# Kernel tuning notes

Hardware: AMD Instinct MI355X
Metric: run time of the kernel (lower is better)

## Reference

```python
import jax, jax.numpy as jnp
import numpy as np

N_NODES = 50000
N_EDGES = 800000
IN_DIM = 128
HID_DIM = 64
OUT_DIM = 40
N_REL = 8


def setup_inputs() -> dict:
    key = jax.random.key(0)
    ks = jax.random.split(key, 12)
    x = jax.random.normal(ks[0], (N_NODES, IN_DIM), dtype=jnp.float32)
    edge_index = jax.random.randint(ks[1], (2, N_EDGES), 0, N_NODES, dtype=jnp.int64)
    edge_type = jax.random.randint(ks[2], (N_EDGES,), 0, N_REL, dtype=jnp.int64)
    s = 0.05
    W1 = jax.random.normal(ks[3], (N_REL, IN_DIM, HID_DIM), dtype=jnp.float32) * s
    root1 = jax.random.normal(ks[4], (IN_DIM, HID_DIM), dtype=jnp.float32) * s
    b1 = jnp.zeros((HID_DIM,), dtype=jnp.float32)
    W2 = jax.random.normal(ks[5], (N_REL, HID_DIM, HID_DIM), dtype=jnp.float32) * s
    root2 = jax.random.normal(ks[6], (HID_DIM, HID_DIM), dtype=jnp.float32) * s
    b2 = jnp.zeros((HID_DIM,), dtype=jnp.float32)
    Wl = jax.random.normal(ks[7], (HID_DIM, OUT_DIM), dtype=jnp.float32) * s
    bl = jnp.zeros((OUT_DIM,), dtype=jnp.float32)
    return {"x": x, "edge_index": edge_index, "edge_type": edge_type,
            "W1": W1, "root1": root1, "b1": b1,
            "W2": W2, "root2": root2, "b2": b2,
            "Wl": Wl, "bl": bl}


def _rgcn_conv(x, W, Wroot, b, src, dst, edge_type):
    # PyG RGCNConv (no bases/blocks, aggr='mean'):
    #   out[i] = sum_r mean_{(j->i) of rel r} (x[j] @ W[r]) + x[i] @ Wroot + b
    N = x.shape[0]
    R = W.shape[0]
    h = jnp.einsum('ni,rio->rno', x, W)        # [R, N, out]
    msgs = h[edge_type, src]                   # [E, out] edge gather
    seg = edge_type * N + dst                  # per (relation, dst) segment
    sums = jax.ops.segment_sum(msgs, seg, num_segments=R * N)
    cnt = jax.ops.segment_sum(jnp.ones((msgs.shape[0],), x.dtype), seg,
                              num_segments=R * N)
    mean = sums / jnp.maximum(cnt, 1.0)[:, None]
    agg = mean.reshape(R, N, -1).sum(axis=0)   # sum over relations
    return agg + x @ Wroot + b


def reference(x, edge_index, edge_type, W1, root1, b1, W2, root2, b2, Wl, bl):
    src, dst = edge_index[0], edge_index[1]
    h = jax.nn.relu(_rgcn_conv(x, W1, root1, b1, src, dst, edge_type))
    # dropout is identity in eval mode
    h = jax.nn.relu(_rgcn_conv(h, W2, root2, b2, src, dst, edge_type))
    logits = h @ Wl + bl
    return jax.nn.log_softmax(logits, axis=1)
```

## Files before the change

kernel.cpp:

```cpp
#include <hip/hip_runtime.h>
#include <hip/hip_bf16.h>
#include <cmath>

#define IN_DIM 128
#define HID 64
#define OUT_DIM 40
#define NREL 8
#define NCOLS 576
#define CAP 64
#define CSTR 16

typedef __attribute__((ext_vector_type(8))) short short8;
typedef __attribute__((ext_vector_type(4))) short short4v;
typedef __attribute__((ext_vector_type(4))) float floatx4;
typedef __attribute__((ext_vector_type(2))) float f32x2;

static __device__ __forceinline__ short f2bf(float f) {
  __hip_bfloat16 h = __float2bfloat16(f);
  return __builtin_bit_cast(short, h);
}
static __device__ __forceinline__ float bflo(unsigned int u) {
  return __int_as_float(u << 16);
}
static __device__ __forceinline__ float bfhi(unsigned int u) {
  return __int_as_float(u & 0xffff0000u);
}
static __device__ __forceinline__ unsigned int packbf(float x, float y) {
  unsigned int lo = (unsigned short)f2bf(x);
  unsigned int hi = (unsigned short)f2bf(y);
  return lo | (hi << 16);
}

__global__ void pack_zero(const float* __restrict__ W1, const float* __restrict__ root1,
                          short* __restrict__ Bt1,
                          const float* __restrict__ W2, const float* __restrict__ root2,
                          short* __restrict__ Bt2,
                          int4* __restrict__ curv, int nz) {
  const int PB1 = (NCOLS * IN_DIM + 255) / 256;
  const int PB2 = (NCOLS * HID + 255) / 256;
  int b = blockIdx.x;
  if (b < PB1) {
    int i = b * 256 + threadIdx.x;
    if (i >= NCOLS * IN_DIM) return;
    int c = i / IN_DIM, k = i % IN_DIM;
    float v = (c < NREL * HID)
      ? W1[((size_t)(c >> 6) * IN_DIM + k) * HID + (c & 63)]
      : root1[(size_t)k * HID + (c - NREL * HID)];
    Bt1[i] = f2bf(v);
  } else if (b < PB1 + PB2) {
    int i = (b - PB1) * 256 + threadIdx.x;
    if (i >= NCOLS * HID) return;
    int c = i / HID, k = i % HID;
    float v = (c < NREL * HID)
      ? W2[((size_t)(c >> 6) * HID + k) * HID + (c & 63)]
      : root2[(size_t)k * HID + (c - NREL * HID)];
    Bt2[i] = f2bf(v);
  } else {
    int i = (b - PB1 - PB2) * 256 + threadIdx.x;
    if (i < nz) curv[i] = make_int4(0, 0, 0, 0);
  }
}

template<int K, int AMODE>
__device__ __forceinline__ void gemm_dev(
    short* As, short* Bs,
    const void* __restrict__ Aptr, const short* __restrict__ Bt,
    const float* __restrict__ bias, short* __restrict__ H,
    unsigned short* __restrict__ AGG, int M, int row0)
{
  constexpr int AST = K + 8;
  int tid = threadIdx.x;
  int wv = tid >> 6, lane = tid & 63;
  int lm = lane & 15, quad = lane >> 4;

  if (AMODE == 0) {
    const float* A = (const float*)Aptr;
    constexpr int CH = K / 4;
    for (int i = tid; i < 64 * CH; i += 256) {
      int r = i / CH, kq = i % CH;
      int gr = row0 + r; if (gr >= M) gr = M - 1;
      float4 v = *(const float4*)(A + (unsigned)(gr * K + kq * 4));
      short4v s;
      s.x = f2bf(v.x); s.y = f2bf(v.y); s.z = f2bf(v.z); s.w = f2bf(v.w);
      *(short4v*)(As + r * AST + kq * 4) = s;
    }
  } else {
    const short* A = (const short*)Aptr;
    constexpr int CH = K / 8;
    for (int i = tid; i < 64 * CH; i += 256) {
      int r = i / CH, ko = i % CH;
      int gr = row0 + r; if (gr >= M) gr = M - 1;
      short8 v = *(const short8*)(A + (unsigned)(gr * K + ko * 8));
      #pragma unroll
      for (int j = 0; j < 8; ++j)
        if ((unsigned short)v[j] & 0x8000u) v[j] = 0;
      *(short8*)(As + r * AST + ko * 8) = v;
    }
  }

  const short* ap = As + (16 * wv + lm) * AST + quad * 8;

  for (int cy = 0; cy < 9; ++cy) {
    constexpr int CB = K / 8;
    for (int i = tid; i < 64 * CB; i += 256) {
      int n = i / CB, ko = i % CB;
      short8 v = *(const short8*)(Bt + (unsigned)((cy * 64 + n) * K + ko * 8));
      *(short8*)(Bs + n * AST + ko * 8) = v;
    }
    __syncthreads();

    floatx4 acc[4] = {{0,0,0,0},{0,0,0,0},{0,0,0,0},{0,0,0,0}};
    #pragma unroll
    for (int ks = 0; ks < K / 32; ++ks) {
      short8 a = *(const short8*)(ap + ks * 32);
      #pragma unroll
      for (int nb = 0; nb < 4; ++nb) {
        short8 b = *(const short8*)(Bs + (nb * 16 + lm) * AST + ks * 32 + quad * 8);
        acc[nb] = __builtin_amdgcn_mfma_f32_16x16x32_bf16(a, b, acc[nb], 0, 0, 0);
      }
    }
    __syncthreads();

    int mbase = row0 + 16 * wv + quad * 4;
    if (cy < 8) {
      #pragma unroll
      for (int nb = 0; nb < 4; ++nb) {
        int col = cy * 64 + nb * 16 + lm;
        #pragma unroll
        for (int r = 0; r < 4; ++r) {
          int mg = mbase + r;
          if (mg < M) H[(unsigned)mg * (NREL * HID) + col] = f2bf(acc[nb][r]);
        }
      }
    } else {
      #pragma unroll
      for (int nb = 0; nb < 4; ++nb) {
        int col = nb * 16 + lm;
        float bv = bias[col];
        #pragma unroll
        for (int r = 0; r < 4; ++r) {
          int mg = mbase + r;
          if (mg < M)
            AGG[(unsigned)mg * HID + col] = (unsigned short)f2bf(acc[nb][r] + bv);
        }
      }
    }
  }
}

__global__ __launch_bounds__(256, 4) void gemm1_scatter(
    const float* __restrict__ A, const short* __restrict__ Bt,
    const float* __restrict__ bias, short* __restrict__ H,
    unsigned short* __restrict__ AGG, int M, int GB,
    const int* __restrict__ src, const int* __restrict__ dst,
    const int* __restrict__ et,
    int* __restrict__ cursor, int* __restrict__ ev, int E)
{
  constexpr int AST = IN_DIM + 8;
  __shared__ short As[64 * AST];
  __shared__ short Bs[64 * AST];
  if ((int)blockIdx.x < GB) {
    gemm_dev<IN_DIM, 0>(As, Bs, A, Bt, bias, H, AGG, M, blockIdx.x * 64);
  } else {
    int e = (blockIdx.x - GB) * 256 + threadIdx.x;
    if (e >= E) return;
    int d = dst[e];
    int pos = atomicAdd(&cursor[d * CSTR], 1);
    if (pos < CAP)
      __builtin_nontemporal_store((src[e] << 3) | et[e], &ev[d * CAP + pos]);
  }
}

__global__ __launch_bounds__(256, 4) void gemm2_mfma(
    const unsigned short* __restrict__ A, const short* __restrict__ Bt,
    const float* __restrict__ bias, short* __restrict__ H,
    unsigned short* __restrict__ AGG, int M)
{
  constexpr int AST = HID + 8;
  __shared__ short As[64 * AST];
  __shared__ short Bs[64 * AST];
  gemm_dev<HID, 1>(As, Bs, A, Bt, bias, H, AGG, M, blockIdx.x * 64);
}

static __device__ __forceinline__ void agg_core(
    const uint2* __restrict__ Hu2, const int* __restrict__ evrow,
    int cnt, int lane, int q, int sub,
    float& a0, float& a1, float& a2, float& a3)
{
  int ew = evrow[lane];
  int t = ew & 7;
  float wt = 0.f;
  #pragma unroll
  for (int r = 0; r < 8; ++r) {
    unsigned long long m = __ballot(lane < cnt && t == r);
    int c = __popcll(m);
    if (t == r) wt = 1.0f / (float)(c > 1 ? c : 1);
  }
  f32x2 A01 = {a0, a1}, A23 = {a2, a3};
  int npass = (cnt + 31) >> 5;
  for (int P = 0; P < npass; ++P) {
    int base = P * 32 + q * 8;
    int ee[8]; float ww[8];
    #pragma unroll
    for (int i = 0; i < 8; ++i) {
      int j = base + i;
      int jj = j < cnt ? j : cnt - 1;
      ee[i] = __shfl(ew, jj, 64);
      float w = __shfl(wt, jj, 64);
      ww[i] = (j < cnt) ? w : 0.f;
    }
    uint2 hv[8];
    #pragma unroll
    for (int i = 0; i < 8; ++i)
      hv[i] = Hu2[(unsigned)ee[i] * 16u + (unsigned)sub];
    #pragma unroll
    for (int i = 0; i < 8; ++i) {
      f32x2 w2 = {ww[i], ww[i]};
      f32x2 h01 = {bflo(hv[i].x), bfhi(hv[i].x)};
      f32x2 h23 = {bflo(hv[i].y), bfhi(hv[i].y)};
      A01 += h01 * w2;
      A23 += h23 * w2;
    }
  }
  a0 = A01.x; a1 = A01.y; a2 = A23.x; a3 = A23.y;
  a0 += __shfl_xor(a0, 16, 64); a0 += __shfl_xor(a0, 32, 64);
  a1 += __shfl_xor(a1, 16, 64); a1 += __shfl_xor(a1, 32, 64);
  a2 += __shfl_xor(a2, 16, 64); a2 += __shfl_xor(a2, 32, 64);
  a3 += __shfl_xor(a3, 16, 64); a3 += __shfl_xor(a3, 32, 64);
}

__global__ __launch_bounds__(256) void csr_agg(
    const short* __restrict__ H, const int* __restrict__ cursor,
    const int* __restrict__ ev, unsigned short* __restrict__ AGG, int N)
{
  int d = blockIdx.x * 4 + (threadIdx.x >> 6);
  if (d >= N) return;
  int lane = threadIdx.x & 63;
  int q = lane >> 4, sub = lane & 15;
  int cnt = cursor[d * CSTR]; if (cnt > CAP) cnt = CAP;
  float a0 = 0.f, a1 = 0.f, a2 = 0.f, a3 = 0.f;
  uint2* aggrow = (uint2*)(AGG + (size_t)d * HID);
  if (q == 0) {
    uint2 iv = aggrow[sub];
    a0 = bflo(iv.x); a1 = bfhi(iv.x); a2 = bflo(iv.y); a3 = bfhi(iv.y);
  }
  if (cnt > 0)
    agg_core((const uint2*)H, ev + d * CAP, cnt, lane, q, sub, a0, a1, a2, a3);
  if (q == 0) {
    uint2 ov;
    ov.x = packbf(a0, a1);
    ov.y = packbf(a2, a3);
    aggrow[sub] = ov;
  }
}

__global__ __launch_bounds__(256) void csr_agg_final(
    const short* __restrict__ H, const int* __restrict__ cursor,
    const int* __restrict__ ev, const unsigned short* __restrict__ AGG,
    const float* __restrict__ Wl, const float* __restrict__ bl,
    float* __restrict__ out, int N)
{
  __shared__ float sWl[HID * OUT_DIM];
  __shared__ float sbl[OUT_DIM];
  __shared__ float sh[4][HID];
  int tid = threadIdx.x;
  for (int i = tid; i < HID * OUT_DIM; i += 256) sWl[i] = Wl[i];
  if (tid < OUT_DIM) sbl[tid] = bl[tid];
  __syncthreads();

  int wv = tid >> 6, lane = tid & 63;
  int q = lane >> 4, sub = lane & 15;
  int d = blockIdx.x * 4 + wv;
  bool valid = d < N;
  int dc = valid ? d : (N - 1);

  int cnt = cursor[dc * CSTR]; if (cnt > CAP) cnt = CAP;
  float a0 = 0.f, a1 = 0.f, a2 = 0.f, a3 = 0.f;
  if (q == 0) {
    uint2 iv = ((const uint2*)(AGG + (size_t)dc * HID))[sub];
    a0 = bflo(iv.x); a1 = bfhi(iv.x); a2 = bflo(iv.y); a3 = bfhi(iv.y);
  }
  if (cnt > 0)
    agg_core((const uint2*)H, ev + dc * CAP, cnt, lane, q, sub, a0, a1, a2, a3);
  if (q == 0) {
    float4 v;
    v.x = fmaxf(a0, 0.f); v.y = fmaxf(a1, 0.f);
    v.z = fmaxf(a2, 0.f); v.w = fmaxf(a3, 0.f);
    *(float4*)(&sh[wv][4 * sub]) = v;
  }
  __syncthreads();

  float logit = -__builtin_inff();
  if (lane < OUT_DIM) {
    float t = sbl[lane];
    #pragma unroll 8
    for (int k = 0; k < HID; ++k) t += sh[wv][k] * sWl[k * OUT_DIM + lane];
    logit = t;
  }
  float m = logit;
  #pragma unroll
  for (int o = 32; o > 0; o >>= 1) m = fmaxf(m, __shfl_xor(m, o, 64));
  float ex = (lane < OUT_DIM) ? expf(logit - m) : 0.f;
  float s = ex;
  #pragma unroll
  for (int o = 32; o > 0; o >>= 1) s += __shfl_xor(s, o, 64);
  if (valid && lane < OUT_DIM)
    out[(size_t)d * OUT_DIM + lane] = logit - m - logf(s);
}

extern "C" void kernel_launch(void* const* d_in, const int* in_sizes, int n_in,
                              void* d_out, int out_size, void* d_ws, size_t ws_size,
                              hipStream_t stream) {
  const float* x     = (const float*)d_in[0];
  const int*   eidx  = (const int*)d_in[1];
  const int*   etype = (const int*)d_in[2];
  const float* W1    = (const float*)d_in[3];
  const float* root1 = (const float*)d_in[4];
  const float* b1    = (const float*)d_in[5];
  const float* W2    = (const float*)d_in[6];
  const float* root2 = (const float*)d_in[7];
  const float* b2    = (const float*)d_in[8];
  const float* Wl    = (const float*)d_in[9];
  const float* bl    = (const float*)d_in[10];

  int N = in_sizes[0] / IN_DIM;
  int E = in_sizes[2];
  const int* srcp = eidx;
  const int* dstp = eidx + E;

  char* ws = (char*)d_ws;
  size_t off = 0;
  auto alloc = [&](size_t bytes) -> char* {
    char* p = ws + off;
    off += (bytes + 255) & ~(size_t)255;
    return p;
  };
  short* Bt1    = (short*)alloc((size_t)NCOLS * IN_DIM * 2);
  short* Bt2    = (short*)alloc((size_t)NCOLS * HID * 2);
  int*   cursor = (int*)alloc((size_t)N * CSTR * 4);
  int*   ev     = (int*)alloc((size_t)N * CAP * 4);
  short* H      = (short*)alloc((size_t)N * NREL * HID * 2);
  unsigned short* AGG1 = (unsigned short*)alloc((size_t)N * HID * 2);
  unsigned short* AGG2 = (unsigned short*)alloc((size_t)N * HID * 2);

  const int PB1 = (NCOLS * IN_DIM + 255) / 256;
  const int PB2 = (NCOLS * HID + 255) / 256;
  int nz = N * CSTR / 4;
  int ZB = (nz + 255) / 256;
  pack_zero<<<PB1 + PB2 + ZB, 256, 0, stream>>>(W1, root1, Bt1, W2, root2, Bt2,
                                                (int4*)cursor, nz);

  int GB = (N + 63) / 64;
  int SB = (E + 255) / 256;
  gemm1_scatter<<<GB + SB, 256, 0, stream>>>(x, Bt1, b1, H, AGG1, N, GB,
                                             srcp, dstp, etype, cursor, ev, E);

  csr_agg<<<(N + 3) / 4, 256, 0, stream>>>(H, cursor, ev, AGG1, N);
  gemm2_mfma<<<GB, 256, 0, stream>>>(AGG1, Bt2, b2, H, AGG2, N);
  csr_agg_final<<<(N + 3) / 4, 256, 0, stream>>>(H, cursor, ev, AGG2,
                                                 Wl, bl, (float*)d_out, N);
}
```

Baseline: 233.3 us.

## Fuse layer-1 aggregation into layer-2 GEMM and precompute edge weight codes

Removes the standalone csr_agg kernel. The second GEMM now gathers neighbours for its own 64-row tile, applies ReLU and writes the aggregated rows straight into shared memory, so the AGG1 round trip through global memory goes away. A new finalize_ev pass packs each edge's per-relation count code into the edge list once. Both aggregation paths then get their mean weights from a small reciprocal lookup table and read edge entries with vector loads, instead of recomputing ballots and shuffles every time. The trade-off is a gather phase with much less parallelism: each wave handles 16 rows serially inside only about 782 GEMM blocks. It also adds an extra kernel launch and a second H buffer, and AGG1 is reused as AGG2.

```diff
diff --git a/kernel.cpp b/kernel.cpp
--- a/kernel.cpp
+++ b/kernel.cpp
@@ -61,41 +61,26 @@
   }
 }
 
-template<int K, int AMODE>
-__device__ __forceinline__ void gemm_dev(
+__device__ __forceinline__ void gemm1_dev(
     short* As, short* Bs,
-    const void* __restrict__ Aptr, const short* __restrict__ Bt,
+    const float* __restrict__ A, const short* __restrict__ Bt,
     const float* __restrict__ bias, short* __restrict__ H,
     unsigned short* __restrict__ AGG, int M, int row0)
 {
+  constexpr int K = IN_DIM;
   constexpr int AST = K + 8;
   int tid = threadIdx.x;
   int wv = tid >> 6, lane = tid & 63;
   int lm = lane & 15, quad = lane >> 4;
 
-  if (AMODE == 0) {
-    const float* A = (const float*)Aptr;
-    constexpr int CH = K / 4;
-    for (int i = tid; i < 64 * CH; i += 256) {
-      int r = i / CH, kq = i % CH;
-      int gr = row0 + r; if (gr >= M) gr = M - 1;
-      float4 v = *(const float4*)(A + (unsigned)(gr * K + kq * 4));
-      short4v s;
-      s.x = f2bf(v.x); s.y = f2bf(v.y); s.z = f2bf(v.z); s.w = f2bf(v.w);
-      *(short4v*)(As + r * AST + kq * 4) = s;
-    }
-  } else {
-    const short* A = (const short*)Aptr;
-    constexpr int CH = K / 8;
-    for (int i = tid; i < 64 * CH; i += 256) {
-      int r = i / CH, ko = i % CH;
-      int gr = row0 + r; if (gr >= M) gr = M - 1;
-      short8 v = *(const short8*)(A + (unsigned)(gr * K + ko * 8));
-      #pragma unroll
-      for (int j = 0; j < 8; ++j)
-        if ((unsigned short)v[j] & 0x8000u) v[j] = 0;
-      *(short8*)(As + r * AST + ko * 8) = v;
-    }
+  constexpr int CH = K / 4;
+  for (int i = tid; i < 64 * CH; i += 256) {
+    int r = i / CH, kq = i % CH;
+    int gr = row0 + r; if (gr >= M) gr = M - 1;
+    float4 v = *(const float4*)(A + (unsigned)(gr * K + kq * 4));
+    short4v s;
+    s.x = f2bf(v.x); s.y = f2bf(v.y); s.z = f2bf(v.z); s.w = f2bf(v.w);
+    *(short4v*)(As + r * AST + kq * 4) = s;
   }
 
   const short* ap = As + (16 * wv + lm) * AST + quad * 8;
@@ -160,7 +145,7 @@
   __shared__ short As[64 * AST];
   __shared__ short Bs[64 * AST];
   if ((int)blockIdx.x < GB) {
-    gemm_dev<IN_DIM, 0>(As, Bs, A, Bt, bias, H, AGG, M, blockIdx.x * 64);
+    gemm1_dev(As, Bs, A, Bt, bias, H, AGG, M, blockIdx.x * 64);
   } else {
     int e = (blockIdx.x - GB) * 256 + threadIdx.x;
     if (e >= E) return;
@@ -171,48 +156,42 @@
   }
 }
 
-__global__ __launch_bounds__(256, 4) void gemm2_mfma(
-    const unsigned short* __restrict__ A, const short* __restrict__ Bt,
-    const float* __restrict__ bias, short* __restrict__ H,
-    unsigned short* __restrict__ AGG, int M)
-{
-  constexpr int AST = HID + 8;
-  __shared__ short As[64 * AST];
-  __shared__ short Bs[64 * AST];
-  gemm_dev<HID, 1>(As, Bs, A, Bt, bias, H, AGG, M, blockIdx.x * 64);
-}
-
-static __device__ __forceinline__ void agg_core(
-    const uint2* __restrict__ Hu2, const int* __restrict__ evrow,
-    int cnt, int lane, int q, int sub,
-    float& a0, float& a1, float& a2, float& a3)
-{
-  int ew = evrow[lane];
-  int t = ew & 7;
-  float wt = 0.f;
+__global__ __launch_bounds__(256) void finalize_ev(
+    const int* __restrict__ cursor, int* __restrict__ ev, int N)
+{
+  int d = blockIdx.x * 4 + (threadIdx.x >> 6);
+  if (d >= N) return;
+  int lane = threadIdx.x & 63;
+  int cnt = cursor[d * CSTR]; if (cnt > CAP) cnt = CAP;
+  int e = (lane < cnt) ? ev[d * CAP + lane] : 0;
+  int t = e & 7;
+  int code = 64;
   #pragma unroll
   for (int r = 0; r < 8; ++r) {
     unsigned long long m = __ballot(lane < cnt && t == r);
     int c = __popcll(m);
-    if (t == r) wt = 1.0f / (float)(c > 1 ? c : 1);
-  }
+    if (lane < cnt && t == r) code = c - 1;
+  }
+  ev[d * CAP + lane] = (e << 7) | code;
+}
+
+static __device__ __forceinline__ void agg_fast(
+    const uint2* __restrict__ Hu2, const int* __restrict__ evrow,
+    int npass, int q, int sub, const float* __restrict__ lut,
+    float& a0, float& a1, float& a2, float& a3)
+{
   f32x2 A01 = {a0, a1}, A23 = {a2, a3};
-  int npass = (cnt + 31) >> 5;
   for (int P = 0; P < npass; ++P) {
-    int base = P * 32 + q * 8;
-    int ee[8]; float ww[8];
+    const int4* pp = (const int4*)(evrow + P * 32 + q * 8);
+    int4 v0 = pp[0], v1 = pp[1];
+    int vv[8] = {v0.x, v0.y, v0.z, v0.w, v1.x, v1.y, v1.z, v1.w};
+    uint2 hv[8];
+    float ww[8];
     #pragma unroll
     for (int i = 0; i < 8; ++i) {
-      int j = base + i;
-      int jj = j < cnt ? j : cnt - 1;
-      ee[i] = __shfl(ew, jj, 64);
-      float w = __shfl(wt, jj, 64);
-      ww[i] = (j < cnt) ? w : 0.f;
-    }
-    uint2 hv[8];
-    #pragma unroll
-    for (int i = 0; i < 8; ++i)
-      hv[i] = Hu2[(unsigned)ee[i] * 16u + (unsigned)sub];
+      hv[i] = Hu2[(unsigned)(vv[i] >> 7) * 16u + (unsigned)sub];
+      ww[i] = lut[vv[i] & 127];
+    }
     #pragma unroll
     for (int i = 0; i < 8; ++i) {
       f32x2 w2 = {ww[i], ww[i]};
@@ -229,28 +208,97 @@
   a3 += __shfl_xor(a3, 16, 64); a3 += __shfl_xor(a3, 32, 64);
 }
 
-__global__ __launch_bounds__(256) void csr_agg(
-    const short* __restrict__ H, const int* __restrict__ cursor,
-    const int* __restrict__ ev, unsigned short* __restrict__ AGG, int N)
-{
-  int d = blockIdx.x * 4 + (threadIdx.x >> 6);
-  if (d >= N) return;
-  int lane = threadIdx.x & 63;
+__global__ __launch_bounds__(256, 4) void gemm2_fused(
+    const unsigned short* __restrict__ AGG1, const int* __restrict__ cursor,
+    const int* __restrict__ ev, const short* __restrict__ H1,
+    const short* __restrict__ Bt, const float* __restrict__ bias,
+    short* __restrict__ H2, unsigned short* __restrict__ AGG2, int M)
+{
+  constexpr int K = HID;
+  constexpr int AST = K + 8;
+  __shared__ short As[64 * AST];
+  __shared__ short Bs[64 * AST];
+  __shared__ float lut[128];
+
+  int tid = threadIdx.x;
+  if (tid < 128) lut[tid] = (tid < 64) ? 1.0f / (float)(tid + 1) : 0.f;
+  __syncthreads();
+
+  int row0 = blockIdx.x * 64;
+  int wv = tid >> 6, lane = tid & 63;
+  int lm = lane & 15, quad = lane >> 4;
   int q = lane >> 4, sub = lane & 15;
-  int cnt = cursor[d * CSTR]; if (cnt > CAP) cnt = CAP;
-  float a0 = 0.f, a1 = 0.f, a2 = 0.f, a3 = 0.f;
-  uint2* aggrow = (uint2*)(AGG + (size_t)d * HID);
-  if (q == 0) {
-    uint2 iv = aggrow[sub];
-    a0 = bflo(iv.x); a1 = bfhi(iv.x); a2 = bflo(iv.y); a3 = bfhi(iv.y);
-  }
-  if (cnt > 0)
-    agg_core((const uint2*)H, ev + d * CAP, cnt, lane, q, sub, a0, a1, a2, a3);
-  if (q == 0) {
-    uint2 ov;
-    ov.x = packbf(a0, a1);
-    ov.y = packbf(a2, a3);
-    aggrow[sub] = ov;
+
+  for (int j = 0; j < 16; ++j) {
+    int r = wv * 16 + j;
+    int d = row0 + r;
+    int dc = d < M ? d : M - 1;
+    int cnt = cursor[dc * CSTR]; if (cnt > CAP) cnt = CAP;
+    float a0 = 0.f, a1 = 0.f, a2 = 0.f, a3 = 0.f;
+    if (q == 0) {
+      uint2 iv = ((const uint2*)(AGG1 + (size_t)dc * HID))[sub];
+      a0 = bflo(iv.x); a1 = bfhi(iv.x); a2 = bflo(iv.y); a3 = bfhi(iv.y);
+    }
+    int npass = (cnt + 31) >> 5;
+    if (npass > 0)
+      agg_fast((const uint2*)H1, ev + dc * CAP, npass, q, sub, lut, a0, a1, a2, a3);
+    if (q == 0) {
+      ushort4 o;
+      o.x = (unsigned short)f2bf(fmaxf(a0, 0.f));
+      o.y = (unsigned short)f2bf(fmaxf(a1, 0.f));
+      o.z = (unsigned short)f2bf(fmaxf(a2, 0.f));
+      o.w = (unsigned short)f2bf(fmaxf(a3, 0.f));
+      *(ushort4*)(As + r * AST + sub * 4) = o;
+    }
+  }
+
+  const short* ap = As + (16 * wv + lm) * AST + quad * 8;
+
+  for (int cy = 0; cy < 9; ++cy) {
+    constexpr int CB = K / 8;
+    for (int i = tid; i < 64 * CB; i += 256) {
+      int n = i / CB, ko = i % CB;
+      short8 v = *(const short8*)(Bt + (unsigned)((cy * 64 + n) * K + ko * 8));
+      *(short8*)(Bs + n * AST + ko * 8) = v;
+    }
+    __syncthreads();
+
+    floatx4 acc[4] = {{0,0,0,0},{0,0,0,0},{0,0,0,0},{0,0,0,0}};
+    #pragma unroll
+    for (int ks = 0; ks < K / 32; ++ks) {
+      short8 a = *(const short8*)(ap + ks * 32);
+      #pragma unroll
+      for (int nb = 0; nb < 4; ++nb) {
+        short8 b = *(const short8*)(Bs + (nb * 16 + lm) * AST + ks * 32 + quad * 8);
+        acc[nb] = __builtin_amdgcn_mfma_f32_16x16x32_bf16(a, b, acc[nb], 0, 0, 0);
+      }
+    }
+    __syncthreads();
+
+    int mbase = row0 + 16 * wv + quad * 4;
+    if (cy < 8) {
+      #pragma unroll
+      for (int nb = 0; nb < 4; ++nb) {
+        int col = cy * 64 + nb * 16 + lm;
+        #pragma unroll
+        for (int r = 0; r < 4; ++r) {
+          int mg = mbase + r;
+          if (mg < M) H2[(unsigned)mg * (NREL * HID) + col] = f2bf(acc[nb][r]);
+        }
+      }
+    } else {
+      #pragma unroll
+      for (int nb = 0; nb < 4; ++nb) {
+        int col = nb * 16 + lm;
+        float bv = bias[col];
+        #pragma unroll
+        for (int r = 0; r < 4; ++r) {
+          int mg = mbase + r;
+          if (mg < M)
+            AGG2[(unsigned)mg * HID + col] = (unsigned short)f2bf(acc[nb][r] + bv);
+        }
+      }
+    }
   }
 }
 
@@ -263,9 +311,11 @@
   __shared__ float sWl[HID * OUT_DIM];
   __shared__ float sbl[OUT_DIM];
   __shared__ float sh[4][HID];
+  __shared__ float lut[128];
   int tid = threadIdx.x;
   for (int i = tid; i < HID * OUT_DIM; i += 256) sWl[i] = Wl[i];
   if (tid < OUT_DIM) sbl[tid] = bl[tid];
+  if (tid < 128) lut[tid] = (tid < 64) ? 1.0f / (float)(tid + 1) : 0.f;
   __syncthreads();
 
   int wv = tid >> 6, lane = tid & 63;
@@ -280,8 +330,9 @@
     uint2 iv = ((const uint2*)(AGG + (size_t)dc * HID))[sub];
     a0 = bflo(iv.x); a1 = bfhi(iv.x); a2 = bflo(iv.y); a3 = bfhi(iv.y);
   }
-  if (cnt > 0)
-    agg_core((const uint2*)H, ev + dc * CAP, cnt, lane, q, sub, a0, a1, a2, a3);
+  int npass = (cnt + 31) >> 5;
+  if (npass > 0)
+    agg_fast((const uint2*)H, ev + dc * CAP, npass, q, sub, lut, a0, a1, a2, a3);
   if (q == 0) {
     float4 v;
     v.x = fmaxf(a0, 0.f); v.y = fmaxf(a1, 0.f);
@@ -339,9 +390,10 @@
   short* Bt2    = (short*)alloc((size_t)NCOLS * HID * 2);
   int*   cursor = (int*)alloc((size_t)N * CSTR * 4);
   int*   ev     = (int*)alloc((size_t)N * CAP * 4);
-  short* H      = (short*)alloc((size_t)N * NREL * HID * 2);
+  short* H1     = (short*)alloc((size_t)N * NREL * HID * 2);
+  short* H2     = (short*)alloc((size_t)N * NREL * HID * 2);
   unsigned short* AGG1 = (unsigned short*)alloc((size_t)N * HID * 2);
-  unsigned short* AGG2 = (unsigned short*)alloc((size_t)N * HID * 2);
+  unsigned short* AGG2 = AGG1;
 
   const int PB1 = (NCOLS * IN_DIM + 255) / 256;
   const int PB2 = (NCOLS * HID + 255) / 256;
@@ -352,11 +404,13 @@
 
   int GB = (N + 63) / 64;
   int SB = (E + 255) / 256;
-  gemm1_scatter<<<GB + SB, 256, 0, stream>>>(x, Bt1, b1, H, AGG1, N, GB,
+  gemm1_scatter<<<GB + SB, 256, 0, stream>>>(x, Bt1, b1, H1, AGG1, N, GB,
                                              srcp, dstp, etype, cursor, ev, E);
 
-  csr_agg<<<(N + 3) / 4, 256, 0, stream>>>(H, cursor, ev, AGG1, N);
-  gemm2_mfma<<<GB, 256, 0, stream>>>(AGG1, Bt2, b2, H, AGG2, N);
-  csr_agg_final<<<(N + 3) / 4, 256, 0, stream>>>(H, cursor, ev, AGG2,
+  finalize_ev<<<(N + 3) / 4, 256, 0, stream>>>(cursor, ev, N);
+
+  gemm2_fused<<<GB, 256, 0, stream>>>(AGG1, cursor, ev, H1, Bt2, b2, H2, AGG2, N);
+
+  csr_agg_final<<<(N + 3) / 4, 256, 0, stream>>>(H2, cursor, ev, AGG2,
                                                  Wl, bl, (float*)d_out, N);
 }
```

Result: no change. 237.6 us (+1.9%).

## Precompute per-edge mean weights in first aggregation and reuse in final pass

Applied to the files above, without the earlier changes.

The first aggregation kernel now computes per-relation counts through ballots and writes them back into the edge list, packed with the gather index as a small code. The final aggregation then reads those packed entries with vector loads and looks up 1/count in a shared-memory table, instead of repeating the ballot and shuffle work. Cursor zeroing moves to hipMemsetAsync, and the two layers now write separate H buffers. The cost is an extra write of the edge list and a second large H allocation, and the packed index field shrinks to 25 bits, which still fits the node and relation count.

```diff
diff --git a/kernel.cpp b/kernel.cpp
--- a/kernel.cpp
+++ b/kernel.cpp
@@ -31,13 +31,11 @@
   return lo | (hi << 16);
 }
 
-__global__ void pack_zero(const float* __restrict__ W1, const float* __restrict__ root1,
-                          short* __restrict__ Bt1,
-                          const float* __restrict__ W2, const float* __restrict__ root2,
-                          short* __restrict__ Bt2,
-                          int4* __restrict__ curv, int nz) {
+__global__ void pack_bt(const float* __restrict__ W1, const float* __restrict__ root1,
+                        short* __restrict__ Bt1,
+                        const float* __restrict__ W2, const float* __restrict__ root2,
+                        short* __restrict__ Bt2) {
   const int PB1 = (NCOLS * IN_DIM + 255) / 256;
-  const int PB2 = (NCOLS * HID + 255) / 256;
   int b = blockIdx.x;
   if (b < PB1) {
     int i = b * 256 + threadIdx.x;
@@ -47,7 +45,7 @@
       ? W1[((size_t)(c >> 6) * IN_DIM + k) * HID + (c & 63)]
       : root1[(size_t)k * HID + (c - NREL * HID)];
     Bt1[i] = f2bf(v);
-  } else if (b < PB1 + PB2) {
+  } else {
     int i = (b - PB1) * 256 + threadIdx.x;
     if (i >= NCOLS * HID) return;
     int c = i / HID, k = i % HID;
@@ -55,9 +53,6 @@
       ? W2[((size_t)(c >> 6) * HID + k) * HID + (c & 63)]
       : root2[(size_t)k * HID + (c - NREL * HID)];
     Bt2[i] = f2bf(v);
-  } else {
-    int i = (b - PB1 - PB2) * 256 + threadIdx.x;
-    if (i < nz) curv[i] = make_int4(0, 0, 0, 0);
   }
 }
 
@@ -182,20 +177,38 @@
   gemm_dev<HID, 1>(As, Bs, A, Bt, bias, H, AGG, M, blockIdx.x * 64);
 }
 
-static __device__ __forceinline__ void agg_core(
-    const uint2* __restrict__ Hu2, const int* __restrict__ evrow,
-    int cnt, int lane, int q, int sub,
-    float& a0, float& a1, float& a2, float& a3)
-{
-  int ew = evrow[lane];
+__global__ __launch_bounds__(256) void csr_agg_fe(
+    const short* __restrict__ H, const int* __restrict__ cursor,
+    int* __restrict__ ev, unsigned short* __restrict__ AGG, int N)
+{
+  int d = blockIdx.x * 4 + (threadIdx.x >> 6);
+  if (d >= N) return;
+  int lane = threadIdx.x & 63;
+  int q = lane >> 4, sub = lane & 15;
+  int cnt = cursor[d * CSTR]; if (cnt > CAP) cnt = CAP;
+  int* evrow = ev + d * CAP;
+
+  int ew = (lane < cnt) ? evrow[lane] : 0;
   int t = ew & 7;
+  int code = 64;
   float wt = 0.f;
   #pragma unroll
   for (int r = 0; r < 8; ++r) {
     unsigned long long m = __ballot(lane < cnt && t == r);
     int c = __popcll(m);
-    if (t == r) wt = 1.0f / (float)(c > 1 ? c : 1);
-  }
+    if (lane < cnt && t == r) { code = c - 1; wt = 1.0f / (float)(c > 0 ? c : 1); }
+  }
+  evrow[lane] = (ew << 7) | code;
+
+  float a0, a1, a2, a3;
+  uint2* aggrow = (uint2*)(AGG + (size_t)d * HID);
+  uint2 iv = aggrow[sub];
+  a0 = (q == 0) ? bflo(iv.x) : 0.f;
+  a1 = (q == 0) ? bfhi(iv.x) : 0.f;
+  a2 = (q == 0) ? bflo(iv.y) : 0.f;
+  a3 = (q == 0) ? bfhi(iv.y) : 0.f;
+
+  const uint2* Hu2 = (const uint2*)H;
   f32x2 A01 = {a0, a1}, A23 = {a2, a3};
   int npass = (cnt + 31) >> 5;
   for (int P = 0; P < npass; ++P) {
@@ -227,25 +240,7 @@
   a1 += __shfl_xor(a1, 16, 64); a1 += __shfl_xor(a1, 32, 64);
   a2 += __shfl_xor(a2, 16, 64); a2 += __shfl_xor(a2, 32, 64);
   a3 += __shfl_xor(a3, 16, 64); a3 += __shfl_xor(a3, 32, 64);
-}
-
-__global__ __launch_bounds__(256) void csr_agg(
-    const short* __restrict__ H, const int* __restrict__ cursor,
-    const int* __restrict__ ev, unsigned short* __restrict__ AGG, int N)
-{
-  int d = blockIdx.x * 4 + (threadIdx.x >> 6);
-  if (d >= N) return;
-  int lane = threadIdx.x & 63;
-  int q = lane >> 4, sub = lane & 15;
-  int cnt = cursor[d * CSTR]; if (cnt > CAP) cnt = CAP;
-  float a0 = 0.f, a1 = 0.f, a2 = 0.f, a3 = 0.f;
-  uint2* aggrow = (uint2*)(AGG + (size_t)d * HID);
-  if (q == 0) {
-    uint2 iv = aggrow[sub];
-    a0 = bflo(iv.x); a1 = bfhi(iv.x); a2 = bflo(iv.y); a3 = bfhi(iv.y);
-  }
-  if (cnt > 0)
-    agg_core((const uint2*)H, ev + d * CAP, cnt, lane, q, sub, a0, a1, a2, a3);
+
   if (q == 0) {
     uint2 ov;
     ov.x = packbf(a0, a1);
@@ -254,6 +249,39 @@
   }
 }
 
+static __device__ __forceinline__ void agg_fast(
+    const uint2* __restrict__ Hu2, const int* __restrict__ evrow,
+    int npass, int q, int sub, const float* __restrict__ lut,
+    float& a0, float& a1, float& a2, float& a3)
+{
+  f32x2 A01 = {a0, a1}, A23 = {a2, a3};
+  for (int P = 0; P < npass; ++P) {
+    const int4* pp = (const int4*)(evrow + P * 32 + q * 8);
+    int4 v0 = pp[0], v1 = pp[1];
+    int vv[8] = {v0.x, v0.y, v0.z, v0.w, v1.x, v1.y, v1.z, v1.w};
+    uint2 hv[8];
+    float ww[8];
+    #pragma unroll
+    for (int i = 0; i < 8; ++i) {
+      hv[i] = Hu2[(unsigned)(vv[i] >> 7) * 16u + (unsigned)sub];
+      ww[i] = lut[vv[i] & 127];
+    }
+    #pragma unroll
+    for (int i = 0; i < 8; ++i) {
+      f32x2 w2 = {ww[i], ww[i]};
+      f32x2 h01 = {bflo(hv[i].x), bfhi(hv[i].x)};
+      f32x2 h23 = {bflo(hv[i].y), bfhi(hv[i].y)};
+      A01 += h01 * w2;
+      A23 += h23 * w2;
+    }
+  }
+  a0 = A01.x; a1 = A01.y; a2 = A23.x; a3 = A23.y;
+  a0 += __shfl_xor(a0, 16, 64); a0 += __shfl_xor(a0, 32, 64);
+  a1 += __shfl_xor(a1, 16, 64); a1 += __shfl_xor(a1, 32, 64);
+  a2 += __shfl_xor(a2, 16, 64); a2 += __shfl_xor(a2, 32, 64);
+  a3 += __shfl_xor(a3, 16, 64); a3 += __shfl_xor(a3, 32, 64);
+}
+
 __global__ __launch_bounds__(256) void csr_agg_final(
     const short* __restrict__ H, const int* __restrict__ cursor,
     const int* __restrict__ ev, const unsigned short* __restrict__ AGG,
@@ -263,11 +291,8 @@
   __shared__ float sWl[HID * OUT_DIM];
   __shared__ float sbl[OUT_DIM];
   __shared__ float sh[4][HID];
+  __shared__ float lut[128];
   int tid = threadIdx.x;
-  for (int i = tid; i < HID * OUT_DIM; i += 256) sWl[i] = Wl[i];
-  if (tid < OUT_DIM) sbl[tid] = bl[tid];
-  __syncthreads();
-
   int wv = tid >> 6, lane = tid & 63;
   int q = lane >> 4, sub = lane & 15;
   int d = blockIdx.x * 4 + wv;
@@ -275,13 +300,20 @@
   int dc = valid ? d : (N - 1);
 
   int cnt = cursor[dc * CSTR]; if (cnt > CAP) cnt = CAP;
+  uint2 iv = ((const uint2*)(AGG + (size_t)dc * HID))[sub];
+
+  for (int i = tid; i < HID * OUT_DIM; i += 256) sWl[i] = Wl[i];
+  if (tid < OUT_DIM) sbl[tid] = bl[tid];
+  if (tid < 128) lut[tid] = (tid < 64) ? 1.0f / (float)(tid + 1) : 0.f;
+  __syncthreads();
+
   float a0 = 0.f, a1 = 0.f, a2 = 0.f, a3 = 0.f;
   if (q == 0) {
-    uint2 iv = ((const uint2*)(AGG + (size_t)dc * HID))[sub];
     a0 = bflo(iv.x); a1 = bfhi(iv.x); a2 = bflo(iv.y); a3 = bfhi(iv.y);
   }
-  if (cnt > 0)
-    agg_core((const uint2*)H, ev + dc * CAP, cnt, lane, q, sub, a0, a1, a2, a3);
+  int npass = (cnt + 31) >> 5;
+  if (npass > 0)
+    agg_fast((const uint2*)H, ev + dc * CAP, npass, q, sub, lut, a0, a1, a2, a3);
   if (q == 0) {
     float4 v;
     v.x = fmaxf(a0, 0.f); v.y = fmaxf(a1, 0.f);
@@ -339,24 +371,26 @@
   short* Bt2    = (short*)alloc((size_t)NCOLS * HID * 2);
   int*   cursor = (int*)alloc((size_t)N * CSTR * 4);
   int*   ev     = (int*)alloc((size_t)N * CAP * 4);
-  short* H      = (short*)alloc((size_t)N * NREL * HID * 2);
+  short* H1     = (short*)alloc((size_t)N * NREL * HID * 2);
+  short* H2     = (short*)alloc((size_t)N * NREL * HID * 2);
   unsigned short* AGG1 = (unsigned short*)alloc((size_t)N * HID * 2);
   unsigned short* AGG2 = (unsigned short*)alloc((size_t)N * HID * 2);
 
+  hipMemsetAsync(cursor, 0, (size_t)N * CSTR * 4, stream);
+
   const int PB1 = (NCOLS * IN_DIM + 255) / 256;
   const int PB2 = (NCOLS * HID + 255) / 256;
-  int nz = N * CSTR / 4;
-  int ZB = (nz + 255) / 256;
-  pack_zero<<<PB1 + PB2 + ZB, 256, 0, stream>>>(W1, root1, Bt1, W2, root2, Bt2,
-                                                (int4*)cursor, nz);
+  pack_bt<<<PB1 + PB2, 256, 0, stream>>>(W1, root1, Bt1, W2, root2, Bt2);
 
   int GB = (N + 63) / 64;
   int SB = (E + 255) / 256;
-  gemm1_scatter<<<GB + SB, 256, 0, stream>>>(x, Bt1, b1, H, AGG1, N, GB,
+  gemm1_scatter<<<GB + SB, 256, 0, stream>>>(x, Bt1, b1, H1, AGG1, N, GB,
                                              srcp, dstp, etype, cursor, ev, E);
 
-  csr_agg<<<(N + 3) / 4, 256, 0, stream>>>(H, cursor, ev, AGG1, N);
-  gemm2_mfma<<<GB, 256, 0, stream>>>(AGG1, Bt2, b2, H, AGG2, N);
-  csr_agg_final<<<(N + 3) / 4, 256, 0, stream>>>(H, cursor, ev, AGG2,
+  csr_agg_fe<<<(N + 3) / 4, 256, 0, stream>>>(H1, cursor, ev, AGG1, N);
+
+  gemm2_mfma<<<GB, 256, 0, stream>>>(AGG1, Bt2, b2, H2, AGG2, N);
+
+  csr_agg_final<<<(N + 3) / 4, 256, 0, stream>>>(H2, cursor, ev, AGG2,
                                                  Wl, bl, (float*)d_out, N);
 }
```

Result: no change. 232.8 us (-0.2%).
